# Performance work log

Hardware: AMD Instinct MI355X
Metric: run time of the kernel (lower is better)

Reference implementation:

```python
import jax, jax.numpy as jnp
import numpy as np

B, S, D, H = 2, 2048, 1024, 16
HD = D // H
E, K = 4, 2              # n_routed_experts, num_experts_per_tok
HID = int(4.0 * D)       # mlp_ratio * d_model
ALPHA = 0.01             # aux (load-balance) loss coefficient
EPS = 1e-5


def _ln(x, g, b):
    m = jnp.mean(x, -1, keepdims=True)
    v = jnp.var(x, -1, keepdims=True)
    return (x - m) * jax.lax.rsqrt(v + EPS) * g + b


def setup_inputs() -> dict:
    key = jax.random.key(0)
    ks = jax.random.split(key, 9)
    s = 0.02
    f32 = jnp.float32
    return {
        "x": jax.random.normal(ks[0], (B, S, D), f32),
        "ln1_g": jnp.ones((D,), f32), "ln1_b": jnp.zeros((D,), f32),
        "Wqkv": jax.random.normal(ks[1], (3 * D, D), f32) * s,
        "bqkv": jnp.zeros((3 * D,), f32),
        "Wo": jax.random.normal(ks[2], (D, D), f32) * s,
        "bo": jnp.zeros((D,), f32),
        "ln2_g": jnp.ones((D,), f32), "ln2_b": jnp.zeros((D,), f32),
        "Wg": jax.random.normal(ks[3], (E, D), f32) * s,            # router (no bias)
        "We_up": jax.random.normal(ks[4], (E, HID, D), f32) * s,
        "be_up": jnp.zeros((E, HID), f32),
        "We_down": jax.random.normal(ks[5], (E, D, HID), f32) * s,
        "be_down": jnp.zeros((E, D), f32),
        "Ws_up": jax.random.normal(ks[6], (HID, D), f32) * s,       # shared expert
        "bs_up": jnp.zeros((HID,), f32),
        "Ws_down": jax.random.normal(ks[7], (D, HID), f32) * s,
        "bs_down": jnp.zeros((D,), f32),
    }


def reference(x, ln1_g, ln1_b, Wqkv, bqkv, Wo, bo, ln2_g, ln2_b,
              Wg, We_up, be_up, We_down, be_down,
              Ws_up, bs_up, Ws_down, bs_down):
    # ---- causal multi-head self-attention (pre-LN) ----
    h = _ln(x, ln1_g, ln1_b)
    qkv = h @ Wqkv.T + bqkv                              # [B,S,3D]
    q, k, v = jnp.split(qkv, 3, axis=-1)
    to_heads = lambda t: t.reshape(B, S, H, HD).transpose(0, 2, 1, 3)
    q, k, v = to_heads(q), to_heads(k), to_heads(v)       # [B,H,S,HD]
    scores = jnp.einsum('bhqd,bhkd->bhqk', q, k) / np.float32(np.sqrt(HD))
    causal = jnp.tril(jnp.ones((S, S), bool))
    scores = jnp.where(causal, scores, jnp.float32(-1e9))
    attn = jax.nn.softmax(scores, axis=-1)
    o = jnp.einsum('bhqk,bhkd->bhqd', attn, v)
    o = o.transpose(0, 2, 1, 3).reshape(B, S, D)
    x = x + (o @ Wo.T + bo)                               # residual 1

    # ---- MoE feed-forward (pre-LN) ----
    T = B * S
    h2 = _ln(x, ln2_g, ln2_b).reshape(T, D)
    logits = h2 @ Wg.T                                    # [T,E]
    probs = jax.nn.softmax(logits, axis=-1)
    topw, topi = jax.lax.top_k(probs, K)                  # [T,K]
    topw = topw / jnp.sum(topw, -1, keepdims=True)        # renormalize top-k

    # dense expert evaluation (faithful math; kernel target is the sparse dispatch)
    up = jax.nn.gelu(jnp.einsum('td,ehd->eth', h2, We_up) + be_up[:, None, :])
    eo = jnp.einsum('eth,edh->etd', up, We_down) + be_down[:, None, :]  # [E,T,D]
    gathered = eo[topi.T, jnp.arange(T)[None, :]]         # [K,T,D]
    y = jnp.einsum('kt,ktd->td', topw.T, gathered)        # combine

    # shared expert (always-on)
    y = y + (jax.nn.gelu(h2 @ Ws_up.T + bs_up) @ Ws_down.T + bs_down)

    # load-balancing auxiliary loss (switch-style)
    assign = jax.nn.one_hot(topi, E, dtype=probs.dtype).sum(1)  # [T,E]
    fi = jnp.mean(assign, 0) / K                          # fraction routed to each expert
    Pi = jnp.mean(probs, 0)                               # mean router prob
    aux = ALPHA * E * jnp.sum(fi * Pi)

    x = x + y.reshape(B, S, D)                            # residual 2
    return aux, x
```

## Files before the change

kernel.cpp:

```cpp
#include <hip/hip_runtime.h>
#include <hip/hip_bf16.h>

#define T_TOK 4096
#define DIM   1024
#define NHEAD 16
#define HDIM  64
#define SEQ   2048
#define NEXP  4
#define HIDD  4096
#define QS    66

typedef short bf16x8 __attribute__((ext_vector_type(8)));
typedef float f32x4  __attribute__((ext_vector_type(4)));

enum { GF_GELU = 1, GF_RESID = 2, GF_SCALE = 4, GF_ACCUM = 8 };

__device__ inline unsigned short f2bf(float f) {
  union { float f; unsigned u; } v; v.f = f;
  unsigned r = v.u + 0x7FFFu + ((v.u >> 16) & 1u);
  return (unsigned short)(r >> 16);
}
__device__ inline int pack2(float a, float b) {
  return (int)((unsigned)f2bf(a) | ((unsigned)f2bf(b) << 16));
}
__device__ inline float gelu_f(float x) {
  float u = 1.5957691216057308f * x * (1.0f + 0.044715f * x * x);
  float w = __expf(u);
  return x - x * __builtin_amdgcn_rcpf(w + 1.0f);
}
__device__ inline void gld_lds16(const unsigned short* g, unsigned short* l) {
  __builtin_amdgcn_global_load_lds(
      (const __attribute__((address_space(1))) void*)g,
      (__attribute__((address_space(3))) void*)l, 16, 0, 0);
}

__global__ __launch_bounds__(256) void cvt_kernel(
    const float* __restrict__ in, unsigned short* __restrict__ out, int n8)
{
  int i = blockIdx.x * 256 + threadIdx.x;
  if (i >= n8) return;
  const float4* p = (const float4*)in + (size_t)i * 2;
  float4 v0 = p[0], v1 = p[1];
  int4 pk = make_int4(pack2(v0.x, v0.y), pack2(v0.z, v0.w),
                      pack2(v1.x, v1.y), pack2(v1.z, v1.w));
  *(int4*)(out + (size_t)i * 8) = pk;
}

__global__ __launch_bounds__(256) void gemm_bf16(
    const unsigned short* __restrict__ A, const unsigned short* __restrict__ W,
    const float* __restrict__ bias, const float* __restrict__ resid,
    const float* __restrict__ scale, float* __restrict__ C,
    float* __restrict__ Cz, unsigned short* __restrict__ C2,
    int M, int N, int Kd, int flags)
{
  __shared__ __align__(16) unsigned short As[128 * 64];
  __shared__ __align__(16) unsigned short Bs[128 * 64];

  const int tid  = threadIdx.x;
  const int wave = tid >> 6, lane = tid & 63;
  const int bm = blockIdx.y, bn = blockIdx.x;
  const int kz = blockIdx.z;
  const int kseg = Kd / gridDim.z;
  if (kz == 1) C = Cz;

  const int srow = lane >> 3;
  const int scol = ((lane & 7) ^ srow) << 3;
  const unsigned short* Ag = A + (size_t)(bm * 128 + wave * 32 + srow) * Kd + scol + (size_t)kz * kseg;
  const unsigned short* Wg = W + (size_t)(bn * 128 + wave * 32 + srow) * Kd + scol + (size_t)kz * kseg;
  unsigned short* AsBase = As + wave * 32 * 64;
  unsigned short* BsBase = Bs + wave * 32 * 64;

  const int wm = wave >> 1, wn = wave & 1;
  const int fr = lane & 15;
  const int fq = lane >> 4;
  const int f7 = fr & 7;

  f32x4 acc[4][4] = {};

  for (int k0 = 0; k0 < kseg; k0 += 64) {
    __syncthreads();
    gld_lds16(Ag + k0,            AsBase);
    gld_lds16(Ag + k0 +  8 * Kd,  AsBase +  8 * 64);
    gld_lds16(Ag + k0 + 16 * Kd,  AsBase + 16 * 64);
    gld_lds16(Ag + k0 + 24 * Kd,  AsBase + 24 * 64);
    gld_lds16(Wg + k0,            BsBase);
    gld_lds16(Wg + k0 +  8 * Kd,  BsBase +  8 * 64);
    gld_lds16(Wg + k0 + 16 * Kd,  BsBase + 16 * 64);
    gld_lds16(Wg + k0 + 24 * Kd,  BsBase + 24 * 64);
    __syncthreads();
#pragma unroll
    for (int ks = 0; ks < 2; ++ks) {
      const int ch = ((ks * 4 + fq) ^ f7) << 3;
      bf16x8 a[4], b[4];
#pragma unroll
      for (int i = 0; i < 4; ++i) {
        a[i] = *(const bf16x8*)&As[(wm * 64 + i * 16 + fr) * 64 + ch];
        b[i] = *(const bf16x8*)&Bs[(wn * 64 + i * 16 + fr) * 64 + ch];
      }
#pragma unroll
      for (int mt = 0; mt < 4; ++mt)
#pragma unroll
        for (int nt = 0; nt < 4; ++nt)
          acc[mt][nt] = __builtin_amdgcn_mfma_f32_16x16x32_bf16(a[mt], b[nt], acc[mt][nt], 0, 0, 0);
    }
  }

#pragma unroll
  for (int mt = 0; mt < 4; ++mt)
#pragma unroll
    for (int nt = 0; nt < 4; ++nt)
#pragma unroll
      for (int r = 0; r < 4; ++r) {
        int row = bm * 128 + wm * 64 + mt * 16 + fq * 4 + r;
        int col = bn * 128 + wn * 64 + nt * 16 + fr;
        float v = acc[mt][nt][r];
        if (bias) v += bias[col];
        if (flags & GF_GELU) v = gelu_f(v);
        if (flags & GF_RESID) v += resid[(size_t)row * N + col];
        if (flags & GF_SCALE) v *= scale[row];
        size_t idx = (size_t)row * N + col;
        if (C) { if (flags & GF_ACCUM) C[idx] += v; else C[idx] = v; }
        if (C2) C2[idx] = f2bf(v);
      }
}

__global__ __launch_bounds__(256) void attn_mfma(
    const unsigned short* __restrict__ qkv, unsigned short* __restrict__ o)
{
  __shared__ __align__(16) unsigned short Qs[64 * QS];
  __shared__ __align__(16) unsigned short Ks[64 * QS];
  __shared__ __align__(16) unsigned short Vt[64 * QS];
  __shared__ __align__(16) unsigned short Ps[64 * QS];

  const int tid  = threadIdx.x;
  const int wave = tid >> 6, lane = tid & 63;
  const int quad = lane >> 4, l15 = lane & 15;
  const int bh = blockIdx.y, b = bh >> 4, h = bh & 15;

  const int srow = tid >> 2;
  const int scol = (tid & 3) << 4;
  const int swcol = srow ^ ((tid & 3) << 3);

  const unsigned short* kvb = qkv + (size_t)b * SEQ * 3072 + 1024 + h * 64 + scol;

  int4 ka, kb, va, vb;

  for (int half = 0; half < 2; ++half) {
    const int qb = half ? (31 - (int)blockIdx.x) : (int)blockIdx.x;
    const int q0 = qb << 6;

    __syncthreads();
    {
      const unsigned short* qp = qkv + ((size_t)(b * SEQ + q0 + srow)) * 3072 + h * 64 + scol;
      *(int4*)&Qs[srow * QS + scol]     = *(const int4*)qp;
      *(int4*)&Qs[srow * QS + scol + 8] = *(const int4*)(qp + 8);
    }
    {
      const unsigned short* kp = kvb + (size_t)srow * 3072;
      ka = *(const int4*)kp;           kb = *(const int4*)(kp + 8);
      va = *(const int4*)(kp + 1024);  vb = *(const int4*)(kp + 1024 + 8);
    }
    __syncthreads();
    bf16x8 qf0 = *(const bf16x8*)&Qs[(wave * 16 + l15) * QS + quad * 8];
    bf16x8 qf1 = *(const bf16x8*)&Qs[(wave * 16 + l15) * QS + 32 + quad * 8];

    f32x4 Oc[4] = {};
    float mr[4] = {-1e30f, -1e30f, -1e30f, -1e30f};
    float ls[4] = {0.f, 0.f, 0.f, 0.f};

    for (int kt = 0; kt <= qb; ++kt) {
      __syncthreads();
      {
        *(int4*)&Ks[srow * QS + scol]     = ka;
        *(int4*)&Ks[srow * QS + scol + 8] = kb;
        unsigned short vs[16];
        *(int4*)&vs[0] = va;
        *(int4*)&vs[8] = vb;
#pragma unroll
        for (int i = 0; i < 16; ++i)
          Vt[(scol + i) * QS + swcol] = vs[i];
      }
      if (kt < qb) {
        const unsigned short* kp = kvb + (size_t)((kt + 1) * 64 + srow) * 3072;
        ka = *(const int4*)kp;           kb = *(const int4*)(kp + 8);
        va = *(const int4*)(kp + 1024);  vb = *(const int4*)(kp + 1024 + 8);
      }
      __syncthreads();

      f32x4 sc[4] = {};
#pragma unroll
      for (int ct = 0; ct < 4; ++ct) {
        bf16x8 k0 = *(const bf16x8*)&Ks[(ct * 16 + l15) * QS + quad * 8];
        bf16x8 k1 = *(const bf16x8*)&Ks[(ct * 16 + l15) * QS + 32 + quad * 8];
        sc[ct] = __builtin_amdgcn_mfma_f32_16x16x32_bf16(qf0, k0, sc[ct], 0, 0, 0);
        sc[ct] = __builtin_amdgcn_mfma_f32_16x16x32_bf16(qf1, k1, sc[ct], 0, 0, 0);
      }

      float sv[4][4];
      const bool diag = (kt == qb);
#pragma unroll
      for (int ct = 0; ct < 4; ++ct)
#pragma unroll
        for (int r = 0; r < 4; ++r) {
          float v = sc[ct][r] * 0.125f;
          if (diag && (ct * 16 + l15) > (wave * 16 + quad * 4 + r)) v = -1e9f;
          sv[ct][r] = v;
        }
      float rm[4], rs[4];
#pragma unroll
      for (int r = 0; r < 4; ++r)
        rm[r] = fmaxf(fmaxf(sv[0][r], sv[1][r]), fmaxf(sv[2][r], sv[3][r]));
#pragma unroll
      for (int m = 1; m < 16; m <<= 1)
#pragma unroll
        for (int r = 0; r < 4; ++r) rm[r] = fmaxf(rm[r], __shfl_xor(rm[r], m, 16));
      float al[4];
#pragma unroll
      for (int r = 0; r < 4; ++r) {
        float nm = fmaxf(mr[r], rm[r]);
        al[r] = __expf(mr[r] - nm);
        mr[r] = nm;
        rs[r] = 0.f;
      }
#pragma unroll
      for (int ct = 0; ct < 4; ++ct)
#pragma unroll
        for (int r = 0; r < 4; ++r) {
          float p = __expf(sv[ct][r] - mr[r]);
          sv[ct][r] = p;
          rs[r] += p;
        }
#pragma unroll
      for (int m = 1; m < 16; m <<= 1)
#pragma unroll
        for (int r = 0; r < 4; ++r) rs[r] += __shfl_xor(rs[r], m, 16);
#pragma unroll
      for (int r = 0; r < 4; ++r) {
        ls[r] = ls[r] * al[r] + rs[r];
        for (int ct = 0; ct < 4; ++ct) Oc[ct][r] *= al[r];
      }
#pragma unroll
      for (int ct = 0; ct < 4; ++ct)
#pragma unroll
        for (int r = 0; r < 4; ++r)
          Ps[(wave * 16 + quad * 4 + r) * QS + ct * 16 + l15] = f2bf(sv[ct][r]);
      bf16x8 pf0 = *(const bf16x8*)&Ps[(wave * 16 + l15) * QS + quad * 8];
      bf16x8 pf1 = *(const bf16x8*)&Ps[(wave * 16 + l15) * QS + 32 + quad * 8];
#pragma unroll
      for (int ct = 0; ct < 4; ++ct) {
        bf16x8 v0 = *(const bf16x8*)&Vt[(ct * 16 + l15) * QS + ((quad ^ ct) << 3)];
        bf16x8 v1 = *(const bf16x8*)&Vt[(ct * 16 + l15) * QS + 32 + ((quad ^ ct) << 3)];
        Oc[ct] = __builtin_amdgcn_mfma_f32_16x16x32_bf16(pf0, v0, Oc[ct], 0, 0, 0);
        Oc[ct] = __builtin_amdgcn_mfma_f32_16x16x32_bf16(pf1, v1, Oc[ct], 0, 0, 0);
      }
    }

#pragma unroll
    for (int r = 0; r < 4; ++r) {
      float inv = 1.0f / ls[r];
      unsigned short* orow = o + ((size_t)(b * SEQ + q0 + wave * 16 + quad * 4 + r)) * DIM + h * 64;
#pragma unroll
      for (int ct = 0; ct < 4; ++ct)
        orow[ct * 16 + l15] = f2bf(Oc[ct][r] * inv);
    }
  }
}

__global__ __launch_bounds__(256) void ln_kernel(
    const float* __restrict__ x, const float* __restrict__ g,
    const float* __restrict__ b, unsigned short* __restrict__ out)
{
  const int t = blockIdx.x, tid = threadIdx.x;
  const float* row = x + (size_t)t * DIM;
  float4 v = *(const float4*)(row + tid * 4);
  float s  = v.x + v.y + v.z + v.w;
  float s2 = v.x * v.x + v.y * v.y + v.z * v.z + v.w * v.w;
  for (int off = 1; off < 64; off <<= 1) {
    s  += __shfl_xor(s, off, 64);
    s2 += __shfl_xor(s2, off, 64);
  }
  __shared__ float red[8];
  const int wave = tid >> 6, lane = tid & 63;
  if (lane == 0) { red[wave] = s; red[4 + wave] = s2; }
  __syncthreads();
  float S  = red[0] + red[1] + red[2] + red[3];
  float S2 = red[4] + red[5] + red[6] + red[7];
  float mean = S * (1.0f / DIM);
  float var  = S2 * (1.0f / DIM) - mean * mean;
  float rstd = rsqrtf(var + 1e-5f);
  float4 gv = *(const float4*)(g + tid * 4);
  float4 bv = *(const float4*)(b + tid * 4);
  float ox = (v.x - mean) * rstd * gv.x + bv.x;
  float oy = (v.y - mean) * rstd * gv.y + bv.y;
  float oz = (v.z - mean) * rstd * gv.z + bv.z;
  float ow = (v.w - mean) * rstd * gv.w + bv.w;
  int2 pk; pk.x = pack2(ox, oy); pk.y = pack2(oz, ow);
  *(int2*)(out + (size_t)t * DIM + tid * 4) = pk;
}

__global__ __launch_bounds__(128) void router_kernel(
    const float* __restrict__ xin, const float* __restrict__ g,
    const float* __restrict__ bb, const float* __restrict__ Wgp,
    float* __restrict__ stab, float* __restrict__ probs4, int* __restrict__ tops)
{
  const int t = blockIdx.x, tid = threadIdx.x;
  const float* row = xin + (size_t)t * DIM;
  float v[8]; float s = 0.f, s2 = 0.f;
#pragma unroll
  for (int k = 0; k < 8; ++k) {
    float u = row[tid + 128 * k];
    v[k] = u; s += u; s2 += u * u;
  }
  for (int off = 1; off < 64; off <<= 1) {
    s  += __shfl_xor(s, off, 64);
    s2 += __shfl_xor(s2, off, 64);
  }
  __shared__ float red[4];
  const int wv = tid >> 6, ln = tid & 63;
  if (ln == 0) { red[wv] = s; red[2 + wv] = s2; }
  __syncthreads();
  float S = red[0] + red[1], S2 = red[2] + red[3];
  float mean = S * (1.0f / DIM);
  float var  = S2 * (1.0f / DIM) - mean * mean;
  float rstd = rsqrtf(var + 1e-5f);
  float p0 = 0, p1 = 0, p2 = 0, p3 = 0;
#pragma unroll
  for (int k = 0; k < 8; ++k) {
    int i = tid + 128 * k;
    float hv = (v[k] - mean) * rstd * g[i] + bb[i];
    p0 += hv * Wgp[i];
    p1 += hv * Wgp[DIM + i];
    p2 += hv * Wgp[2 * DIM + i];
    p3 += hv * Wgp[3 * DIM + i];
  }
  __shared__ float sm[4][128];
  sm[0][tid] = p0; sm[1][tid] = p1; sm[2][tid] = p2; sm[3][tid] = p3;
  __syncthreads();
  for (int sft = 64; sft > 0; sft >>= 1) {
    if (tid < sft)
      for (int e = 0; e < 4; ++e) sm[e][tid] += sm[e][tid + sft];
    __syncthreads();
  }
  if (tid == 0) {
    float l[4] = { sm[0][0], sm[1][0], sm[2][0], sm[3][0] };
    float m = fmaxf(fmaxf(l[0], l[1]), fmaxf(l[2], l[3]));
    float pr[4]; float sum = 0.f;
    for (int e = 0; e < 4; ++e) { pr[e] = __expf(l[e] - m); sum += pr[e]; }
    for (int e = 0; e < 4; ++e) pr[e] /= sum;
    int i0 = 0;
    for (int e = 1; e < 4; ++e) if (pr[e] > pr[i0]) i0 = e;
    int i1 = -1;
    for (int e = 0; e < 4; ++e) if (e != i0 && (i1 < 0 || pr[e] > pr[i1])) i1 = e;
    float wsum = pr[i0] + pr[i1];
    for (int e = 0; e < 4; ++e)
      stab[(size_t)e * T_TOK + t] = (e == i0) ? pr[i0] / wsum : (e == i1) ? pr[i1] / wsum : 0.f;
    ((float4*)probs4)[t] = make_float4(pr[0], pr[1], pr[2], pr[3]);
    tops[t] = i0 | (i1 << 2);
  }
}

__global__ __launch_bounds__(256) void moe_stats_kernel(
    const float* __restrict__ probs4, const int* __restrict__ tops,
    float* __restrict__ outaux)
{
  const int tid = threadIdx.x;
  float pi0 = 0, pi1 = 0, pi2 = 0, pi3 = 0;
  float fi0 = 0, fi1 = 0, fi2 = 0, fi3 = 0;
  for (int t = tid; t < T_TOK; t += 256) {
    float4 p = ((const float4*)probs4)[t];
    pi0 += p.x; pi1 += p.y; pi2 += p.z; pi3 += p.w;
    int ii = tops[t];
    int a = ii & 3, b = (ii >> 2) & 3;
    fi0 += (a == 0 ? 1.f : 0.f) + (b == 0 ? 1.f : 0.f);
    fi1 += (a == 1 ? 1.f : 0.f) + (b == 1 ? 1.f : 0.f);
    fi2 += (a == 2 ? 1.f : 0.f) + (b == 2 ? 1.f : 0.f);
    fi3 += (a == 3 ? 1.f : 0.f) + (b == 3 ? 1.f : 0.f);
  }
  for (int off = 1; off < 64; off <<= 1) {
    pi0 += __shfl_xor(pi0, off, 64); pi1 += __shfl_xor(pi1, off, 64);
    pi2 += __shfl_xor(pi2, off, 64); pi3 += __shfl_xor(pi3, off, 64);
    fi0 += __shfl_xor(fi0, off, 64); fi1 += __shfl_xor(fi1, off, 64);
    fi2 += __shfl_xor(fi2, off, 64); fi3 += __shfl_xor(fi3, off, 64);
  }
  __shared__ float red[8][4];
  const int wv = tid >> 6, ln = tid & 63;
  if (ln == 0) {
    red[0][wv] = pi0; red[1][wv] = pi1; red[2][wv] = pi2; red[3][wv] = pi3;
    red[4][wv] = fi0; red[5][wv] = fi1; red[6][wv] = fi2; red[7][wv] = fi3;
  }
  __syncthreads();
  if (tid == 0) {
    float P[4], F[4];
    for (int e = 0; e < 4; ++e) {
      P[e] = red[e][0] + red[e][1] + red[e][2] + red[e][3];
      F[e] = red[4 + e][0] + red[4 + e][1] + red[4 + e][2] + red[4 + e][3];
    }
    float sacc = F[0] * P[0] + F[1] * P[1] + F[2] * P[2] + F[3] * P[3];
    outaux[0] = 0.01f * 4.0f * sacc / (2.0f * (float)T_TOK * (float)T_TOK);
  }
}

__global__ __launch_bounds__(256) void init_y_kernel(
    const float* __restrict__ bs_dn, const float* __restrict__ be_dn,
    const float* __restrict__ stab, float* __restrict__ y, float* __restrict__ y2)
{
  const int t = blockIdx.x, c = threadIdx.x;
  float s0 = stab[t], s1 = stab[T_TOK + t], s2 = stab[2 * T_TOK + t], s3 = stab[3 * T_TOK + t];
  float4 acc = ((const float4*)bs_dn)[c];
  float4 b0 = ((const float4*)(be_dn + 0 * DIM))[c];
  float4 b1 = ((const float4*)(be_dn + 1 * DIM))[c];
  float4 b2 = ((const float4*)(be_dn + 2 * DIM))[c];
  float4 b3 = ((const float4*)(be_dn + 3 * DIM))[c];
  acc.x += s0 * b0.x + s1 * b1.x + s2 * b2.x + s3 * b3.x;
  acc.y += s0 * b0.y + s1 * b1.y + s2 * b2.y + s3 * b3.y;
  acc.z += s0 * b0.z + s1 * b1.z + s2 * b2.z + s3 * b3.z;
  acc.w += s0 * b0.w + s1 * b1.w + s2 * b2.w + s3 * b3.w;
  ((float4*)(y + (size_t)t * DIM))[c] = acc;
  ((float4*)(y2 + (size_t)t * DIM))[c] = make_float4(0.f, 0.f, 0.f, 0.f);
}

__global__ __launch_bounds__(256) void add3_kernel(
    const float* __restrict__ a, const float* __restrict__ b,
    const float* __restrict__ c, float* __restrict__ out, int n)
{
  int i = blockIdx.x * 256 + threadIdx.x;
  if (i < n) out[i] = a[i] + b[i] + c[i];
}

extern "C" void kernel_launch(void* const* d_in, const int* in_sizes, int n_in,
                              void* d_out, int out_size, void* d_ws, size_t ws_size,
                              hipStream_t stream)
{
  const float* x      = (const float*)d_in[0];
  const float* ln1_g  = (const float*)d_in[1];
  const float* ln1_b  = (const float*)d_in[2];
  const float* Wqkv   = (const float*)d_in[3];
  const float* bqkv   = (const float*)d_in[4];
  const float* Wo     = (const float*)d_in[5];
  const float* bo     = (const float*)d_in[6];
  const float* ln2_g  = (const float*)d_in[7];
  const float* ln2_b  = (const float*)d_in[8];
  const float* Wg     = (const float*)d_in[9];
  const float* We_up  = (const float*)d_in[10];
  const float* be_up  = (const float*)d_in[11];
  const float* We_dn  = (const float*)d_in[12];
  const float* be_dn  = (const float*)d_in[13];
  const float* Ws_up  = (const float*)d_in[14];
  const float* bs_up  = (const float*)d_in[15];
  const float* Ws_dn  = (const float*)d_in[16];
  const float* bs_dn  = (const float*)d_in[17];

  float* out = (float*)d_out;
  const size_t TD = (size_t)T_TOK * DIM;

  char* w = (char*)d_ws;
  float* x1 = (float*)w;  w += TD * 4;
  float* y  = (float*)w;
  unsigned short* o_bf = (unsigned short*)y;
  w += TD * 4;
  float* y2 = (float*)w;  w += TD * 4;
  unsigned short* pool = (unsigned short*)w;
  unsigned short* qkv_bf = pool;
  unsigned short* up_bf  = pool;
  w += (size_t)T_TOK * HIDD * 2;
  unsigned short* h_bf = (unsigned short*)w;  w += TD * 2;
  unsigned short* P1   = (unsigned short*)w;  w += (size_t)HIDD * DIM * 2;
  unsigned short* P2   = (unsigned short*)w;  w += (size_t)HIDD * DIM * 2;
  float* stab = (float*)w;  w += (size_t)NEXP * T_TOK * 4;
  float* probs4 = (float*)w; w += (size_t)T_TOK * 4 * 4;
  int*   tops   = (int*)w;   w += (size_t)T_TOK * 4;

  auto cvt = [&](const float* src, unsigned short* dst, int n) {
    cvt_kernel<<<(n / 8 + 255) / 256, 256, 0, stream>>>(src, dst, n / 8);
  };

  cvt(Wqkv, P1, 3 * DIM * DIM);
  ln_kernel<<<T_TOK, 256, 0, stream>>>(x, ln1_g, ln1_b, h_bf);
  gemm_bf16<<<dim3(3072 / 128, T_TOK / 128), 256, 0, stream>>>(
      h_bf, P1, bqkv, nullptr, nullptr, nullptr, nullptr, qkv_bf, T_TOK, 3072, DIM, 0);
  attn_mfma<<<dim3(16, 2 * NHEAD), 256, 0, stream>>>(qkv_bf, o_bf);
  cvt(Wo, P2, DIM * DIM);
  gemm_bf16<<<dim3(DIM / 128, T_TOK / 128), 256, 0, stream>>>(
      o_bf, P2, bo, x, nullptr, x1, nullptr, nullptr, T_TOK, DIM, DIM, GF_RESID);
  ln_kernel<<<T_TOK, 256, 0, stream>>>(x1, ln2_g, ln2_b, h_bf);
  router_kernel<<<T_TOK, 128, 0, stream>>>(x1, ln2_g, ln2_b, Wg, stab, probs4, tops);
  moe_stats_kernel<<<1, 256, 0, stream>>>(probs4, tops, out);
  init_y_kernel<<<T_TOK, 256, 0, stream>>>(bs_dn, be_dn, stab, y, y2);
  cvt(Ws_up, P1, HIDD * DIM);
  gemm_bf16<<<dim3(HIDD / 128, T_TOK / 128), 256, 0, stream>>>(
      h_bf, P1, bs_up, nullptr, nullptr, nullptr, nullptr, up_bf, T_TOK, HIDD, DIM, GF_GELU);
  cvt(Ws_dn, P2, DIM * HIDD);
  gemm_bf16<<<dim3(DIM / 128, T_TOK / 128, 2), 256, 0, stream>>>(
      up_bf, P2, nullptr, nullptr, nullptr, y, y2, nullptr, T_TOK, DIM, HIDD, GF_ACCUM);
  for (int e = 0; e < NEXP; ++e) {
    cvt(We_up + (size_t)e * HIDD * DIM, P1, HIDD * DIM);
    gemm_bf16<<<dim3(HIDD / 128, T_TOK / 128), 256, 0, stream>>>(
        h_bf, P1, be_up + (size_t)e * HIDD,
        nullptr, stab + (size_t)e * T_TOK, nullptr, nullptr, up_bf,
        T_TOK, HIDD, DIM, GF_GELU | GF_SCALE);
    cvt(We_dn + (size_t)e * DIM * HIDD, P2, DIM * HIDD);
    gemm_bf16<<<dim3(DIM / 128, T_TOK / 128, 2), 256, 0, stream>>>(
        up_bf, P2, nullptr, nullptr, nullptr, y, y2, nullptr,
        T_TOK, DIM, HIDD, GF_ACCUM);
  }
  add3_kernel<<<(int)(TD / 256), 256, 0, stream>>>(x1, y, y2, out + 1, (int)TD);
}
```

Before: 1.232 ms.

## Add 256x256-tile bf16 GEMM with double-buffered LDS for QKV and up-projections

```diff
diff --git a/kernel.cpp b/kernel.cpp
--- a/kernel.cpp
+++ b/kernel.cpp
@@ -44,6 +44,140 @@
   int4 pk = make_int4(pack2(v0.x, v0.y), pack2(v0.z, v0.w),
                       pack2(v1.x, v1.y), pack2(v1.z, v1.w));
   *(int4*)(out + (size_t)i * 8) = pk;
+}
+
+__global__ __launch_bounds__(512, 2) void gemm256(
+    const unsigned short* __restrict__ A, const unsigned short* __restrict__ W,
+    const float* __restrict__ bias, const float* __restrict__ scale,
+    unsigned short* __restrict__ C2, int N, int Kd, int flags)
+{
+  __shared__ __align__(16) unsigned short Abuf[2][2][256 * 32];
+  __shared__ __align__(16) unsigned short Bbuf[2][2][256 * 32];
+
+  const int tid  = threadIdx.x;
+  const int wave = tid >> 6, lane = tid & 63;
+
+  const int nwg  = gridDim.x * gridDim.y;
+  const int flat = blockIdx.y * gridDim.x + blockIdx.x;
+  const int swz  = (flat & 7) * (nwg >> 3) + (flat >> 3);
+  const int bn = swz % gridDim.x, bm = swz / gridDim.x;
+
+  const int sr = lane >> 2;
+  const int sc = lane & 3;
+  const int gcol = (sc ^ (sr & 3)) << 3;
+  const unsigned short* Ag = A + ((size_t)(bm * 256 + wave * 32 + sr)) * Kd + gcol;
+  const unsigned short* Wg = W + ((size_t)(bn * 256 + wave * 32 + sr)) * Kd + gcol;
+
+  const int wm = wave >> 2, wn = wave & 3;
+  const int fr = lane & 15, fq = lane >> 4;
+  const int fx = (fq ^ (fr & 3)) << 3;
+
+  f32x4 acc[8][4] = {};
+  const int NT = Kd / 64;
+
+  {
+    const unsigned short* a0 = Ag;
+    const unsigned short* b0 = Wg;
+    gld_lds16(a0,           &Abuf[0][0][(wave * 32) * 32]);
+    gld_lds16(a0 + 16 * Kd, &Abuf[0][0][(wave * 32 + 16) * 32]);
+    gld_lds16(b0,           &Bbuf[0][0][(wave * 32) * 32]);
+    gld_lds16(b0 + 16 * Kd, &Bbuf[0][0][(wave * 32 + 16) * 32]);
+    gld_lds16(a0 + 32,           &Abuf[0][1][(wave * 32) * 32]);
+    gld_lds16(a0 + 32 + 16 * Kd, &Abuf[0][1][(wave * 32 + 16) * 32]);
+    gld_lds16(b0 + 32,           &Bbuf[0][1][(wave * 32) * 32]);
+    gld_lds16(b0 + 32 + 16 * Kd, &Bbuf[0][1][(wave * 32 + 16) * 32]);
+  }
+
+  for (int t = 0; t < NT; ++t) {
+    const int buf = t & 1, nb = buf ^ 1;
+    const bool more = (t + 1 < NT);
+    const int nk0 = (t + 1) * 64;
+    bf16x8 a[8], b0, b1;
+
+    asm volatile("s_waitcnt vmcnt(4)" ::: "memory");
+    __builtin_amdgcn_s_barrier();
+#pragma unroll
+    for (int m = 0; m < 8; ++m)
+      a[m] = *(const bf16x8*)&Abuf[buf][0][(wm * 128 + m * 16 + fr) * 32 + fx];
+    b0 = *(const bf16x8*)&Bbuf[buf][0][(wn * 64 +  0 + fr) * 32 + fx];
+    b1 = *(const bf16x8*)&Bbuf[buf][0][(wn * 64 + 16 + fr) * 32 + fx];
+    if (more) {
+      const unsigned short* s0 = Ag + nk0;
+      gld_lds16(s0,           &Abuf[nb][0][(wave * 32) * 32]);
+      gld_lds16(s0 + 16 * Kd, &Abuf[nb][0][(wave * 32 + 16) * 32]);
+    }
+    __builtin_amdgcn_s_setprio(1);
+#pragma unroll
+    for (int m = 0; m < 8; ++m) {
+      acc[m][0] = __builtin_amdgcn_mfma_f32_16x16x32_bf16(a[m], b0, acc[m][0], 0, 0, 0);
+      acc[m][1] = __builtin_amdgcn_mfma_f32_16x16x32_bf16(a[m], b1, acc[m][1], 0, 0, 0);
+    }
+    __builtin_amdgcn_s_setprio(0);
+
+    b0 = *(const bf16x8*)&Bbuf[buf][0][(wn * 64 + 32 + fr) * 32 + fx];
+    b1 = *(const bf16x8*)&Bbuf[buf][0][(wn * 64 + 48 + fr) * 32 + fx];
+    if (more) {
+      const unsigned short* s0 = Wg + nk0;
+      gld_lds16(s0,           &Bbuf[nb][0][(wave * 32) * 32]);
+      gld_lds16(s0 + 16 * Kd, &Bbuf[nb][0][(wave * 32 + 16) * 32]);
+    }
+    __builtin_amdgcn_s_setprio(1);
+#pragma unroll
+    for (int m = 0; m < 8; ++m) {
+      acc[m][2] = __builtin_amdgcn_mfma_f32_16x16x32_bf16(a[m], b0, acc[m][2], 0, 0, 0);
+      acc[m][3] = __builtin_amdgcn_mfma_f32_16x16x32_bf16(a[m], b1, acc[m][3], 0, 0, 0);
+    }
+    __builtin_amdgcn_s_setprio(0);
+
+    asm volatile("s_waitcnt vmcnt(4)" ::: "memory");
+    __builtin_amdgcn_s_barrier();
+#pragma unroll
+    for (int m = 0; m < 8; ++m)
+      a[m] = *(const bf16x8*)&Abuf[buf][1][(wm * 128 + m * 16 + fr) * 32 + fx];
+    b0 = *(const bf16x8*)&Bbuf[buf][1][(wn * 64 +  0 + fr) * 32 + fx];
+    b1 = *(const bf16x8*)&Bbuf[buf][1][(wn * 64 + 16 + fr) * 32 + fx];
+    if (more) {
+      const unsigned short* s0 = Ag + nk0 + 32;
+      gld_lds16(s0,           &Abuf[nb][1][(wave * 32) * 32]);
+      gld_lds16(s0 + 16 * Kd, &Abuf[nb][1][(wave * 32 + 16) * 32]);
+    }
+    __builtin_amdgcn_s_setprio(1);
+#pragma unroll
+    for (int m = 0; m < 8; ++m) {
+      acc[m][0] = __builtin_amdgcn_mfma_f32_16x16x32_bf16(a[m], b0, acc[m][0], 0, 0, 0);
+      acc[m][1] = __builtin_amdgcn_mfma_f32_16x16x32_bf16(a[m], b1, acc[m][1], 0, 0, 0);
+    }
+    __builtin_amdgcn_s_setprio(0);
+
+    b0 = *(const bf16x8*)&Bbuf[buf][1][(wn * 64 + 32 + fr) * 32 + fx];
+    b1 = *(const bf16x8*)&Bbuf[buf][1][(wn * 64 + 48 + fr) * 32 + fx];
+    if (more) {
+      const unsigned short* s0 = Wg + nk0 + 32;
+      gld_lds16(s0,           &Bbuf[nb][1][(wave * 32) * 32]);
+      gld_lds16(s0 + 16 * Kd, &Bbuf[nb][1][(wave * 32 + 16) * 32]);
+    }
+    __builtin_amdgcn_s_setprio(1);
+#pragma unroll
+    for (int m = 0; m < 8; ++m) {
+      acc[m][2] = __builtin_amdgcn_mfma_f32_16x16x32_bf16(a[m], b0, acc[m][2], 0, 0, 0);
+      acc[m][3] = __builtin_amdgcn_mfma_f32_16x16x32_bf16(a[m], b1, acc[m][3], 0, 0, 0);
+    }
+    __builtin_amdgcn_s_setprio(0);
+  }
+
+#pragma unroll
+  for (int m = 0; m < 8; ++m)
+#pragma unroll
+    for (int n = 0; n < 4; ++n)
+#pragma unroll
+      for (int r = 0; r < 4; ++r) {
+        int row = bm * 256 + wm * 128 + m * 16 + fq * 4 + r;
+        int col = bn * 256 + wn * 64 + n * 16 + fr;
+        float v = acc[m][n][r] + bias[col];
+        if (flags & GF_GELU) v = gelu_f(v);
+        if (flags & GF_SCALE) v *= scale[row];
+        C2[(size_t)row * N + col] = f2bf(v);
+      }
 }
 
 __global__ __launch_bounds__(256) void gemm_bf16(
@@ -476,8 +610,8 @@
 
   cvt(Wqkv, P1, 3 * DIM * DIM);
   ln_kernel<<<T_TOK, 256, 0, stream>>>(x, ln1_g, ln1_b, h_bf);
-  gemm_bf16<<<dim3(3072 / 128, T_TOK / 128), 256, 0, stream>>>(
-      h_bf, P1, bqkv, nullptr, nullptr, nullptr, nullptr, qkv_bf, T_TOK, 3072, DIM, 0);
+  gemm256<<<dim3(3072 / 256, T_TOK / 256), 512, 0, stream>>>(
+      h_bf, P1, bqkv, nullptr, qkv_bf, 3072, DIM, 0);
   attn_mfma<<<dim3(16, 2 * NHEAD), 256, 0, stream>>>(qkv_bf, o_bf);
   cvt(Wo, P2, DIM * DIM);
   gemm_bf16<<<dim3(DIM / 128, T_TOK / 128), 256, 0, stream>>>(
@@ -487,17 +621,16 @@
   moe_stats_kernel<<<1, 256, 0, stream>>>(probs4, tops, out);
   init_y_kernel<<<T_TOK, 256, 0, stream>>>(bs_dn, be_dn, stab, y, y2);
   cvt(Ws_up, P1, HIDD * DIM);
-  gemm_bf16<<<dim3(HIDD / 128, T_TOK / 128), 256, 0, stream>>>(
-      h_bf, P1, bs_up, nullptr, nullptr, nullptr, nullptr, up_bf, T_TOK, HIDD, DIM, GF_GELU);
+  gemm256<<<dim3(HIDD / 256, T_TOK / 256), 512, 0, stream>>>(
+      h_bf, P1, bs_up, nullptr, up_bf, HIDD, DIM, GF_GELU);
   cvt(Ws_dn, P2, DIM * HIDD);
   gemm_bf16<<<dim3(DIM / 128, T_TOK / 128, 2), 256, 0, stream>>>(
       up_bf, P2, nullptr, nullptr, nullptr, y, y2, nullptr, T_TOK, DIM, HIDD, GF_ACCUM);
   for (int e = 0; e < NEXP; ++e) {
     cvt(We_up + (size_t)e * HIDD * DIM, P1, HIDD * DIM);
-    gemm_bf16<<<dim3(HIDD / 128, T_TOK / 128), 256, 0, stream>>>(
-        h_bf, P1, be_up + (size_t)e * HIDD,
-        nullptr, stab + (size_t)e * T_TOK, nullptr, nullptr, up_bf,
-        T_TOK, HIDD, DIM, GF_GELU | GF_SCALE);
+    gemm256<<<dim3(HIDD / 256, T_TOK / 256), 512, 0, stream>>>(
+        h_bf, P1, be_up + (size_t)e * HIDD, stab + (size_t)e * T_TOK, up_bf,
+        HIDD, DIM, GF_GELU | GF_SCALE);
     cvt(We_dn + (size_t)e * DIM * HIDD, P2, DIM * HIDD);
     gemm_bf16<<<dim3(DIM / 128, T_TOK / 128, 2), 256, 0, stream>>>(
         up_bf, P2, nullptr, nullptr, nullptr, y, y2, nullptr,
```

Result: faster. 1.038 ms (-15.7%).
